# Performance work log

Measured on AMD Instinct MI355X. Metric: run time of the kernel, lower is better.

## Reference

```python
import jax, jax.numpy as jnp
import numpy as np

H = 32        # query heads
D = 128       # head size
HID = H * D   # 4096
B = 4
S = 1024
T = B * S
NSLOTS = 16384
THETA = 10000.0


def _rope(x, cos, sin):
    # x: [T, ..., D]; cos/sin: [T, D//2] -> broadcast over head dims
    half = x.shape[-1] // 2
    while cos.ndim < x.ndim:
        cos = cos[:, None]
        sin = sin[:, None]
    x1, x2 = x[..., :half], x[..., half:]
    return jnp.concatenate([x1 * cos - x2 * sin, x2 * cos + x1 * sin], axis=-1)


def setup_inputs() -> dict:
    key = jax.random.key(0)
    ks = jax.random.split(key, 6)
    hidden_states = jax.random.normal(ks[0], (T, HID), jnp.float32)
    # rotary tables from real positions (repeat per sequence in the batch)
    pos = jnp.tile(jnp.arange(S, dtype=jnp.float32), B)          # [T]
    inv_freq = 1.0 / (THETA ** (jnp.arange(0, D, 2, dtype=jnp.float32) / D))  # [D/2]
    ang = pos[:, None] * inv_freq[None, :]                        # [T, D/2]
    cos, sin = jnp.cos(ang), jnp.sin(ang)
    qkv_w = jax.random.normal(ks[1], (HID, HID + 2 * D), jnp.float32) * 0.02
    qkv_b = jax.random.normal(ks[2], (HID + 2 * D,), jnp.float32) * 0.02
    dense_w = jax.random.normal(ks[3], (HID, HID), jnp.float32) * 0.02
    dense_b = jax.random.normal(ks[4], (HID,), jnp.float32) * 0.02
    k_cache = jnp.zeros((NSLOTS, D), jnp.float32)
    v_cache = jnp.zeros((NSLOTS, D), jnp.float32)
    slots = jnp.arange(T, dtype=jnp.int32)
    return {"hidden_states": hidden_states, "cos": cos, "sin": sin,
            "k_cache": k_cache, "v_cache": v_cache,
            "qkv_w": qkv_w, "qkv_b": qkv_b, "dense_w": dense_w,
            "dense_b": dense_b, "slots": slots, "batch_size": B}


def reference(hidden_states, cos, sin, k_cache, v_cache,
              qkv_w, qkv_b, dense_w, dense_b, slots, batch_size):
    scale = D ** -0.5
    qkv = hidden_states @ qkv_w + qkv_b                  # [T, H*D + 2D]
    q = qkv[:, :HID].reshape(T, H, D)                    # [T,H,D]
    kv = qkv[:, HID:].reshape(T, 2, D)                   # MQA: 1 kv head
    k, v = kv[:, 0], kv[:, 1]                            # [T,D]
    q = _rope(q, cos, sin)
    k = _rope(k, cos, sin)
    # KV-cache scatter store
    k_cache = k_cache.at[slots].set(k)
    v_cache = v_cache.at[slots].set(v)
    # prefill varlen causal attention (uniform lengths -> [B,S] layout)
    qb = q.reshape(batch_size, S, H, D)
    kb = k.reshape(batch_size, S, D)
    vb = v.reshape(batch_size, S, D)
    scores = jnp.einsum('bqhd,bkd->bhqk', qb, kb) * scale
    causal = jnp.tril(jnp.ones((S, S), bool))
    scores = jnp.where(causal[None, None], scores, jnp.float32(-1e30))
    probs = jax.nn.softmax(scores, axis=-1)
    attn = jnp.einsum('bhqk,bkd->bqhd', probs, vb).reshape(T, HID)
    out = attn @ dense_w + dense_b                       # [T, HID]
    return out, k_cache, v_cache
```

## Files before the change

### kernel.cpp

```cpp
#include <hip/hip_runtime.h>

#define H_   32
#define D_   128
#define HID_ 4096
#define B_   4
#define S_   1024
#define T_   4096
#define NSLOTS_ 16384
#define NQKV_ 4352

typedef __attribute__((ext_vector_type(8))) __bf16 bf16x8;
typedef __attribute__((ext_vector_type(4))) __bf16 bf16x4;
typedef __attribute__((ext_vector_type(4))) float  f32x4;

__device__ __forceinline__ void gld_lds16(const __bf16* g, __bf16* l)
{
    __builtin_amdgcn_global_load_lds(
        (const __attribute__((address_space(1))) void*)g,
        (__attribute__((address_space(3))) void*)l, 16, 0, 0);
}

__global__ __launch_bounds__(256) void cast_bf16_kernel(
    const float* __restrict__ in, __bf16* __restrict__ out, int n4)
{
    int i = blockIdx.x * 256 + threadIdx.x;
    if (i < n4) {
        f32x4 v = ((const f32x4*)in)[i];
        bf16x4 o;
        o[0] = (__bf16)v[0]; o[1] = (__bf16)v[1];
        o[2] = (__bf16)v[2]; o[3] = (__bf16)v[3];
        ((bf16x4*)out)[i] = o;
    }
}

__global__ __launch_bounds__(256) void transpose_cast_kernel(
    const float* __restrict__ in, __bf16* __restrict__ out, int R, int C)
{
    __shared__ float tile[32][33];
    int c0 = blockIdx.x * 32, r0 = blockIdx.y * 32;
    int tx = threadIdx.x;
    int ty = threadIdx.y;
#pragma unroll
    for (int j = 0; j < 32; j += 8)
        tile[ty + j][tx] = in[(size_t)(r0 + ty + j) * C + c0 + tx];
    __syncthreads();
#pragma unroll
    for (int j = 0; j < 32; j += 8)
        out[(size_t)(c0 + ty + j) * R + r0 + tx] = (__bf16)tile[tx][ty + j];
}

#define GBK 32
__global__ __launch_bounds__(256) void gemm_bf16_kernel(
    const __bf16* __restrict__ A, const __bf16* __restrict__ Bt,
    const float* __restrict__ bias, float* __restrict__ C,
    int M, int N, int K)
{
    __shared__ __bf16 sA[128][GBK];
    __shared__ __bf16 sB[128][GBK];

    const int tid  = threadIdx.x;
    const int lane = tid & 63;
    const int wave = tid >> 6;
    const int wm   = wave >> 1;
    const int wn   = wave & 1;
    const int col  = lane & 15;
    const int quad = lane >> 4;
    const int bm = blockIdx.y * 128;
    const int bn = blockIdx.x * 128;

    f32x4 acc[4][4];
#pragma unroll
    for (int mt = 0; mt < 4; ++mt)
#pragma unroll
        for (int nt = 0; nt < 4; ++nt)
#pragma unroll
            for (int r = 0; r < 4; ++r) acc[mt][nt][r] = 0.f;

    const int srow = wave * 32 + (lane >> 2);
    const int scol = (lane & 3) * 8;
    const __bf16* gA0 = A  + (size_t)(bm + srow) * K + scol;
    const __bf16* gA1 = A  + (size_t)(bm + srow + 16) * K + scol;
    const __bf16* gB0 = Bt + (size_t)(bn + srow) * K + scol;
    const __bf16* gB1 = Bt + (size_t)(bn + srow + 16) * K + scol;
    __bf16* lA0 = &sA[wave * 32][0];
    __bf16* lA1 = &sA[wave * 32 + 16][0];
    __bf16* lB0 = &sB[wave * 32][0];
    __bf16* lB1 = &sB[wave * 32 + 16][0];

    for (int k0 = 0; k0 < K; k0 += GBK) {
        __syncthreads();
        gld_lds16(gA0 + k0, lA0);
        gld_lds16(gA1 + k0, lA1);
        gld_lds16(gB0 + k0, lB0);
        gld_lds16(gB1 + k0, lB1);
        __syncthreads();

        bf16x8 af[4], bf[4];
#pragma unroll
        for (int mt = 0; mt < 4; ++mt)
            af[mt] = *(const bf16x8*)&sA[wm * 64 + mt * 16 + col][quad * 8];
#pragma unroll
        for (int nt = 0; nt < 4; ++nt)
            bf[nt] = *(const bf16x8*)&sB[wn * 64 + nt * 16 + col][quad * 8];
#pragma unroll
        for (int mt = 0; mt < 4; ++mt)
#pragma unroll
            for (int nt = 0; nt < 4; ++nt)
                acc[mt][nt] = __builtin_amdgcn_mfma_f32_16x16x32_bf16(
                    af[mt], bf[nt], acc[mt][nt], 0, 0, 0);
    }

#pragma unroll
    for (int mt = 0; mt < 4; ++mt) {
#pragma unroll
        for (int nt = 0; nt < 4; ++nt) {
            int r0 = bm + wm * 64 + mt * 16 + quad * 4;
            int c0 = bn + wn * 64 + nt * 16 + col;
            float bv = bias[c0];
#pragma unroll
            for (int r = 0; r < 4; ++r)
                C[(size_t)(r0 + r) * N + c0] = acc[mt][nt][r] + bv;
        }
    }
}

__global__ __launch_bounds__(256) void rope_scatter_kernel(
    const float* __restrict__ qkv, const float* __restrict__ cosb,
    const float* __restrict__ sinb, const int* __restrict__ slots,
    __bf16* __restrict__ q16, __bf16* __restrict__ k16, __bf16* __restrict__ v16,
    float* __restrict__ kcache, float* __restrict__ vcache)
{
    const int t = blockIdx.x;
    const int tid = threadIdx.x;
    const float* row = qkv + (size_t)t * NQKV_;
    const float* cr = cosb + (size_t)t * 64;
    const float* sr = sinb + (size_t)t * 64;
    const int slot = slots[t];

#pragma unroll
    for (int i = 0; i < 8; ++i) {
        int p = tid + 256 * i;
        int h = p >> 6;
        int d = p & 63;
        float x1 = row[h * 128 + d];
        float x2 = row[h * 128 + 64 + d];
        float c = cr[d], s = sr[d];
        q16[(size_t)t * HID_ + h * 128 + d]      = (__bf16)(x1 * c - x2 * s);
        q16[(size_t)t * HID_ + h * 128 + 64 + d] = (__bf16)(x2 * c + x1 * s);
    }
    if (tid < 64) {
        int d = tid;
        float x1 = row[HID_ + d];
        float x2 = row[HID_ + 64 + d];
        float c = cr[d], s = sr[d];
        float o1 = x1 * c - x2 * s;
        float o2 = x2 * c + x1 * s;
        kcache[(size_t)slot * D_ + d]      = o1;
        kcache[(size_t)slot * D_ + 64 + d] = o2;
        k16[(size_t)t * D_ + d]      = (__bf16)o1;
        k16[(size_t)t * D_ + 64 + d] = (__bf16)o2;
    }
    if (tid < 128) {
        float v = row[HID_ + 128 + tid];
        vcache[(size_t)slot * D_ + tid] = v;
        v16[(size_t)t * D_ + tid] = (__bf16)v;
    }
}

__global__ __launch_bounds__(256) void attn_kernel(
    const __bf16* __restrict__ Q, const __bf16* __restrict__ Kc,
    const __bf16* __restrict__ Vc, __bf16* __restrict__ O)
{
    __shared__ __bf16 sK[64][136];
    __shared__ __bf16 sVt[128][72];
    __shared__ __bf16 sP[4][32][72];

    const int h  = blockIdx.y;
    const int b  = blockIdx.z;
    const int tid = threadIdx.x, lane = tid & 63, wave = tid >> 6;
    const int col = lane & 15, quad = lane >> 4;
    const int tbase = b * S_;
    const float scale = 0.08838834764831845f;

    for (int half = 0; half < 2; ++half) {
        const int qt = half ? (7 - blockIdx.x) : blockIdx.x;
        const int qb = qt * 128;

        bf16x8 aq[2][4];
#pragma unroll
        for (int mt = 0; mt < 2; ++mt)
#pragma unroll
            for (int ks = 0; ks < 4; ++ks)
                aq[mt][ks] = *(const bf16x8*)&Q[(size_t)(tbase + qb + wave * 32 + mt * 16 + col) * HID_
                                                + h * 128 + ks * 32 + quad * 8];

        f32x4 o[2][8];
#pragma unroll
        for (int mt = 0; mt < 2; ++mt)
#pragma unroll
            for (int nd = 0; nd < 8; ++nd)
#pragma unroll
                for (int r = 0; r < 4; ++r) o[mt][nd][r] = 0.f;
        float m_i[2][4], l_i[2][4];
#pragma unroll
        for (int mt = 0; mt < 2; ++mt)
#pragma unroll
            for (int r = 0; r < 4; ++r) { m_i[mt][r] = -3.0e38f; l_i[mt][r] = 0.f; }

        const int ntiles = qt * 2 + 2;
        for (int kt = 0; kt < ntiles; ++kt) {
            const int kb = kt * 64;
            __syncthreads();
#pragma unroll
            for (int i = 0; i < 4; ++i) {
                int c = tid + i * 256;
                int srow = c >> 4;
                int d0 = (c & 15) * 8;
                *(uint4*)&sK[srow][d0] = *(const uint4*)&Kc[(size_t)(tbase + kb + srow) * D_ + d0];
            }
#pragma unroll
            for (int i = 0; i < 4; ++i) {
                int c = tid + i * 256;
                int srow = c & 63;
                int d0 = (c >> 6) * 8;
                bf16x8 v = *(const bf16x8*)&Vc[(size_t)(tbase + kb + srow) * D_ + d0];
#pragma unroll
                for (int j = 0; j < 8; ++j) sVt[d0 + j][srow] = v[j];
            }
            __syncthreads();

            f32x4 sc[2][4];
#pragma unroll
            for (int mt = 0; mt < 2; ++mt)
#pragma unroll
                for (int nt = 0; nt < 4; ++nt)
#pragma unroll
                    for (int r = 0; r < 4; ++r) sc[mt][nt][r] = 0.f;
#pragma unroll
            for (int ks = 0; ks < 4; ++ks) {
                bf16x8 bk[4];
#pragma unroll
                for (int nt = 0; nt < 4; ++nt)
                    bk[nt] = *(const bf16x8*)&sK[nt * 16 + col][ks * 32 + quad * 8];
#pragma unroll
                for (int mt = 0; mt < 2; ++mt)
#pragma unroll
                    for (int nt = 0; nt < 4; ++nt)
                        sc[mt][nt] = __builtin_amdgcn_mfma_f32_16x16x32_bf16(
                            aq[mt][ks], bk[nt], sc[mt][nt], 0, 0, 0);
            }

#pragma unroll
            for (int mt = 0; mt < 2; ++mt) {
#pragma unroll
                for (int r = 0; r < 4; ++r) {
                    int qrow = qb + wave * 32 + mt * 16 + quad * 4 + r;
#pragma unroll
                    for (int nt = 0; nt < 4; ++nt) {
                        float v = sc[mt][nt][r] * scale;
                        int kcol = kb + nt * 16 + col;
                        sc[mt][nt][r] = (kcol > qrow) ? -3.0e38f : v;
                    }
                    float mx = sc[mt][0][r];
#pragma unroll
                    for (int nt = 1; nt < 4; ++nt) mx = fmaxf(mx, sc[mt][nt][r]);
#pragma unroll
                    for (int x = 1; x < 16; x <<= 1) mx = fmaxf(mx, __shfl_xor(mx, x, 64));
                    float mnew = fmaxf(m_i[mt][r], mx);
                    float alpha = __expf(m_i[mt][r] - mnew);
                    m_i[mt][r] = mnew;
                    float rs = 0.f;
#pragma unroll
                    for (int nt = 0; nt < 4; ++nt) {
                        float p = __expf(sc[mt][nt][r] - mnew);
                        sc[mt][nt][r] = p;
                        rs += p;
                    }
#pragma unroll
                    for (int x = 1; x < 16; x <<= 1) rs += __shfl_xor(rs, x, 64);
                    l_i[mt][r] = l_i[mt][r] * alpha + rs;
#pragma unroll
                    for (int nd = 0; nd < 8; ++nd) o[mt][nd][r] *= alpha;
                }
            }

#pragma unroll
            for (int mt = 0; mt < 2; ++mt)
#pragma unroll
                for (int nt = 0; nt < 4; ++nt)
#pragma unroll
                    for (int r = 0; r < 4; ++r)
                        sP[wave][mt * 16 + quad * 4 + r][nt * 16 + col] = (__bf16)sc[mt][nt][r];

#pragma unroll
            for (int ks2 = 0; ks2 < 2; ++ks2) {
                bf16x8 ap[2];
#pragma unroll
                for (int mt = 0; mt < 2; ++mt)
                    ap[mt] = *(const bf16x8*)&sP[wave][mt * 16 + col][ks2 * 32 + quad * 8];
#pragma unroll
                for (int nd = 0; nd < 8; ++nd) {
                    bf16x8 bv = *(const bf16x8*)&sVt[nd * 16 + col][ks2 * 32 + quad * 8];
#pragma unroll
                    for (int mt = 0; mt < 2; ++mt)
                        o[mt][nd] = __builtin_amdgcn_mfma_f32_16x16x32_bf16(
                            ap[mt], bv, o[mt][nd], 0, 0, 0);
                }
            }
        }

#pragma unroll
        for (int mt = 0; mt < 2; ++mt) {
#pragma unroll
            for (int r = 0; r < 4; ++r) {
                int t = tbase + qb + wave * 32 + mt * 16 + quad * 4 + r;
                float inv_l = 1.f / l_i[mt][r];
#pragma unroll
                for (int nd = 0; nd < 8; ++nd)
                    O[(size_t)t * HID_ + h * 128 + nd * 16 + col] = (__bf16)(o[mt][nd][r] * inv_l);
            }
        }
    }
}

extern "C" void kernel_launch(void* const* d_in, const int* in_sizes, int n_in,
                              void* d_out, int out_size, void* d_ws, size_t ws_size,
                              hipStream_t stream)
{
    const float* hidden  = (const float*)d_in[0];
    const float* cosb    = (const float*)d_in[1];
    const float* sinb    = (const float*)d_in[2];
    const float* kc_in   = (const float*)d_in[3];
    const float* vc_in   = (const float*)d_in[4];
    const float* qkv_w   = (const float*)d_in[5];
    const float* qkv_b   = (const float*)d_in[6];
    const float* dense_w = (const float*)d_in[7];
    const float* dense_b = (const float*)d_in[8];
    const int*   slots   = (const int*)d_in[9];

    float* out    = (float*)d_out;
    float* kc_out = out + (size_t)T_ * HID_;
    float* vc_out = kc_out + (size_t)NSLOTS_ * D_;

    char* ws = (char*)d_ws;
    __bf16* A16 = (__bf16*)(ws);
    __bf16* W1T = (__bf16*)(ws + 33554432);
    float*  QKV = (float*)(ws + 69206016);
    __bf16* W2T = (__bf16*)(ws + 69206016);
    __bf16* Q16 = (__bf16*)d_out;
    __bf16* K16 = (__bf16*)((char*)d_out + 33554432);
    __bf16* V16 = (__bf16*)((char*)d_out + 34603008);

    cast_bf16_kernel<<<(T_ * HID_ / 4 + 255) / 256, 256, 0, stream>>>(hidden, A16, T_ * HID_ / 4);
    transpose_cast_kernel<<<dim3(NQKV_ / 32, HID_ / 32), dim3(32, 8), 0, stream>>>(qkv_w, W1T, HID_, NQKV_);
    gemm_bf16_kernel<<<dim3(NQKV_ / 128, T_ / 128), 256, 0, stream>>>(A16, W1T, qkv_b, QKV, T_, NQKV_, HID_);
    hipMemcpyAsync(kc_out, kc_in, (size_t)NSLOTS_ * D_ * 4, hipMemcpyDeviceToDevice, stream);
    hipMemcpyAsync(vc_out, vc_in, (size_t)NSLOTS_ * D_ * 4, hipMemcpyDeviceToDevice, stream);
    rope_scatter_kernel<<<T_, 256, 0, stream>>>(QKV, cosb, sinb, slots, Q16, K16, V16, kc_out, vc_out);
    transpose_cast_kernel<<<dim3(HID_ / 32, HID_ / 32), dim3(32, 8), 0, stream>>>(dense_w, W2T, HID_, HID_);
    attn_kernel<<<dim3(4, H_, B_), 256, 0, stream>>>(Q16, K16, V16, A16);
    gemm_bf16_kernel<<<dim3(HID_ / 128, T_ / 128), 256, 0, stream>>>(A16, W2T, dense_b, out, T_, HID_, HID_);
}
```

Before: 823.1 us.

## Replace 128x128 GEMM with pipelined 256x256 tile kernel using swizzled LDS

Both projection GEMMs now use a 512-thread kernel with 256x256 output tiles and 64-wide K steps. Global-to-LDS loads are double-buffered and staged in quarter chunks ahead of compute, with an XOR swizzle to avoid LDS bank conflicts. Explicit waitcnt, barriers and setprio interleave loads with MFMA work. The aim is more data reuse per byte loaded and latency hiding, at the cost of more registers (32 accumulators), 64KB LDS, and fragile hand-written synchronisation.

```diff
diff --git a/kernel.cpp b/kernel.cpp
--- a/kernel.cpp
+++ b/kernel.cpp
@@ -49,77 +49,128 @@
         out[(size_t)(c0 + ty + j) * R + r0 + tx] = (__bf16)tile[tx][ty + j];
 }
 
-#define GBK 32
-__global__ __launch_bounds__(256) void gemm_bf16_kernel(
+
+#define SB()    __builtin_amdgcn_sched_barrier(0)
+#define BAR()   __builtin_amdgcn_s_barrier()
+#define LGKM0() asm volatile("s_waitcnt lgkmcnt(0)" ::: "memory")
+
+#define LOAD_A(MH, KK)                                                          \
+    _Pragma("unroll")                                                           \
+    for (int m = 0; m < 4; ++m)                                                 \
+        afr[m] = *(const bf16x8*)&lds[buf][KK][(wm * 128 + ((MH)*4 + m) * 16 + col) * 32 + pbE];
+
+#define MFMA_QUAD(MH, KK)                                                       \
+    __builtin_amdgcn_s_setprio(1);                                              \
+    _Pragma("unroll")                                                           \
+    for (int m = 0; m < 4; ++m) {                                               \
+        _Pragma("unroll")                                                       \
+        for (int n = 0; n < 4; ++n)                                             \
+            acc[(MH)*4 + m][n] = __builtin_amdgcn_mfma_f32_16x16x32_bf16(       \
+                afr[m], bfr[KK][n], acc[(MH)*4 + m][n], 0, 0, 0);               \
+    }                                                                           \
+    __builtin_amdgcn_s_setprio(0);
+
+__global__ __launch_bounds__(512, 2) void gemm256_kernel(
     const __bf16* __restrict__ A, const __bf16* __restrict__ Bt,
     const float* __restrict__ bias, float* __restrict__ C,
     int M, int N, int K)
 {
-    __shared__ __bf16 sA[128][GBK];
-    __shared__ __bf16 sB[128][GBK];
+    __shared__ __bf16 lds[2][4][8192];
 
     const int tid  = threadIdx.x;
     const int lane = tid & 63;
     const int wave = tid >> 6;
-    const int wm   = wave >> 1;
-    const int wn   = wave & 1;
+    const int wm   = wave >> 2;
+    const int wn   = wave & 3;
     const int col  = lane & 15;
     const int quad = lane >> 4;
-    const int bm = blockIdx.y * 128;
-    const int bn = blockIdx.x * 128;
-
-    f32x4 acc[4][4];
-#pragma unroll
-    for (int mt = 0; mt < 4; ++mt)
-#pragma unroll
-        for (int nt = 0; nt < 4; ++nt)
-#pragma unroll
-            for (int r = 0; r < 4; ++r) acc[mt][nt][r] = 0.f;
-
-    const int srow = wave * 32 + (lane >> 2);
-    const int scol = (lane & 3) * 8;
-    const __bf16* gA0 = A  + (size_t)(bm + srow) * K + scol;
-    const __bf16* gA1 = A  + (size_t)(bm + srow + 16) * K + scol;
-    const __bf16* gB0 = Bt + (size_t)(bn + srow) * K + scol;
-    const __bf16* gB1 = Bt + (size_t)(bn + srow + 16) * K + scol;
-    __bf16* lA0 = &sA[wave * 32][0];
-    __bf16* lA1 = &sA[wave * 32 + 16][0];
-    __bf16* lB0 = &sB[wave * 32][0];
-    __bf16* lB1 = &sB[wave * 32 + 16][0];
-
-    for (int k0 = 0; k0 < K; k0 += GBK) {
-        __syncthreads();
-        gld_lds16(gA0 + k0, lA0);
-        gld_lds16(gA1 + k0, lA1);
-        gld_lds16(gB0 + k0, lB0);
-        gld_lds16(gB1 + k0, lB1);
-        __syncthreads();
-
-        bf16x8 af[4], bf[4];
-#pragma unroll
-        for (int mt = 0; mt < 4; ++mt)
-            af[mt] = *(const bf16x8*)&sA[wm * 64 + mt * 16 + col][quad * 8];
-#pragma unroll
-        for (int nt = 0; nt < 4; ++nt)
-            bf[nt] = *(const bf16x8*)&sB[wn * 64 + nt * 16 + col][quad * 8];
-#pragma unroll
-        for (int mt = 0; mt < 4; ++mt)
-#pragma unroll
-            for (int nt = 0; nt < 4; ++nt)
-                acc[mt][nt] = __builtin_amdgcn_mfma_f32_16x16x32_bf16(
-                    af[mt], bf[nt], acc[mt][nt], 0, 0, 0);
-    }
-
-#pragma unroll
-    for (int mt = 0; mt < 4; ++mt) {
-#pragma unroll
-        for (int nt = 0; nt < 4; ++nt) {
-            int r0 = bm + wm * 64 + mt * 16 + quad * 4;
-            int c0 = bn + wn * 64 + nt * 16 + col;
-            float bv = bias[c0];
+    const int pbE  = (quad ^ ((lane >> 1) & 3)) * 8;
+    const int bm   = blockIdx.y * 256;
+    const int bn   = blockIdx.x * 256;
+    const int nk   = K >> 6;
+    const int nitems = nk << 2;
+
+    const int sR = wave * 32 + (lane >> 2);
+    const int sb = ((lane & 3) ^ ((lane >> 3) & 3)) * 8;
+    const __bf16* gA = A  + (size_t)(bm + sR) * K + sb;
+    const __bf16* gB = Bt + (size_t)(bn + sR) * K + sb;
+
+    f32x4 acc[8][4];
+#pragma unroll
+    for (int m = 0; m < 8; ++m)
+#pragma unroll
+        for (int n = 0; n < 4; ++n)
+#pragma unroll
+            for (int r = 0; r < 4; ++r) acc[m][n][r] = 0.f;
+
+    auto stage = [&](int idx) {
+        if (idx >= nitems) return;
+        const int j   = idx >> 2;
+        const int sel = idx & 3;
+        const int reg = sel ^ 2;
+        const __bf16* g = (sel & 2) ? gA : gB;
+        const size_t koff = (size_t)j * 64 + (size_t)(sel & 1) * 32;
+        __bf16* l = &lds[j & 1][reg][wave * 1024];
+        gld_lds16(g + koff, l);
+        gld_lds16(g + koff + (size_t)16 * K, l + 512);
+    };
+
+    stage(0); stage(1); stage(2); stage(3);
+    asm volatile("s_waitcnt vmcnt(4)" ::: "memory");
+    stage(4); stage(5); stage(6);
+    asm volatile("s_waitcnt vmcnt(6)" ::: "memory");
+    BAR();
+    SB();
+
+    for (int k = 0; k < nk; ++k) {
+        const int buf = k & 1;
+        bf16x8 bfr[2][4];
+        bf16x8 afr[4];
+
+#pragma unroll
+        for (int kk = 0; kk < 2; ++kk)
+#pragma unroll
+            for (int n = 0; n < 4; ++n)
+                bfr[kk][n] = *(const bf16x8*)&lds[buf][2 + kk][(wn * 64 + n * 16 + col) * 32 + pbE];
+        LOAD_A(0, 0)
+        stage(4 * k + 7);
+        SB(); BAR(); LGKM0(); SB();
+        MFMA_QUAD(0, 0)
+        SB(); BAR(); SB();
+
+        LOAD_A(1, 0)
+        stage(4 * k + 8);
+        SB(); BAR(); LGKM0(); SB();
+        MFMA_QUAD(1, 0)
+        SB(); BAR(); SB();
+
+        LOAD_A(0, 1)
+        stage(4 * k + 9);
+        SB(); BAR(); LGKM0(); SB();
+        MFMA_QUAD(0, 1)
+        SB(); BAR(); SB();
+
+        LOAD_A(1, 1)
+        stage(4 * k + 10);
+        SB(); BAR(); LGKM0(); SB();
+        MFMA_QUAD(1, 1)
+        SB();
+        if (k < nk - 2) asm volatile("s_waitcnt vmcnt(6)" ::: "memory");
+        else            asm volatile("s_waitcnt vmcnt(0)" ::: "memory");
+        BAR();
+        SB();
+    }
+
+#pragma unroll
+    for (int m = 0; m < 8; ++m) {
+#pragma unroll
+        for (int n = 0; n < 4; ++n) {
+            const int r0 = bm + wm * 128 + m * 16 + quad * 4;
+            const int c0 = bn + wn * 64 + n * 16 + col;
+            const float bv = bias[c0];
 #pragma unroll
             for (int r = 0; r < 4; ++r)
-                C[(size_t)(r0 + r) * N + c0] = acc[mt][nt][r] + bv;
+                C[(size_t)(r0 + r) * N + c0] = acc[m][n][r] + bv;
         }
     }
 }
@@ -353,11 +404,11 @@
 
     cast_bf16_kernel<<<(T_ * HID_ / 4 + 255) / 256, 256, 0, stream>>>(hidden, A16, T_ * HID_ / 4);
     transpose_cast_kernel<<<dim3(NQKV_ / 32, HID_ / 32), dim3(32, 8), 0, stream>>>(qkv_w, W1T, HID_, NQKV_);
-    gemm_bf16_kernel<<<dim3(NQKV_ / 128, T_ / 128), 256, 0, stream>>>(A16, W1T, qkv_b, QKV, T_, NQKV_, HID_);
+    gemm256_kernel<<<dim3(NQKV_ / 256, T_ / 256), 512, 0, stream>>>(A16, W1T, qkv_b, QKV, T_, NQKV_, HID_);
     hipMemcpyAsync(kc_out, kc_in, (size_t)NSLOTS_ * D_ * 4, hipMemcpyDeviceToDevice, stream);
     hipMemcpyAsync(vc_out, vc_in, (size_t)NSLOTS_ * D_ * 4, hipMemcpyDeviceToDevice, stream);
     rope_scatter_kernel<<<T_, 256, 0, stream>>>(QKV, cosb, sinb, slots, Q16, K16, V16, kc_out, vc_out);
     transpose_cast_kernel<<<dim3(HID_ / 32, HID_ / 32), dim3(32, 8), 0, stream>>>(dense_w, W2T, HID_, HID_);
     attn_kernel<<<dim3(4, H_, B_), 256, 0, stream>>>(Q16, K16, V16, A16);
-    gemm_bf16_kernel<<<dim3(HID_ / 128, T_ / 128), 256, 0, stream>>>(A16, W2T, dense_b, out, T_, HID_, HID_);
-}
+    gemm256_kernel<<<dim3(HID_ / 256, T_ / 256), 512, 0, stream>>>(A16, W2T, dense_b, out, T_, HID_, HID_);
+}
```

Result: faster. 744.5 us (-9.6%).

## Double-buffer GEMM LDS tiles with swizzle and XCD-aware block remap

Applied to the files above, without the earlier changes.

Rewrites the bf16 GEMM to double-buffer its shared-memory tiles, issuing the global-to-LDS loads for step k+2 while MFMAs run on step k, with explicit waitcnt and barrier scheduling. It adds an XOR swizzle on the LDS layout to cut bank conflicts, and remaps the 1D grid so consecutive tiles are spread across the 8 XCDs for better L2 locality. The aim is to hide global-load latency and the two full barriers per K step of the old loop. The hand-placed inline asm waits and sched barriers are fragile, and the grid remap assumes the block count divides by 8.

```diff
diff --git a/kernel.cpp b/kernel.cpp
--- a/kernel.cpp
+++ b/kernel.cpp
@@ -20,6 +20,18 @@
         (__attribute__((address_space(3))) void*)l, 16, 0, 0);
 }
 
+__device__ __forceinline__ bf16x8 ds_read_b128a(const __bf16* p)
+{
+    bf16x8 r;
+    unsigned a = (unsigned)(size_t)(const __attribute__((address_space(3))) __bf16*)p;
+    asm volatile("ds_read_b128 %0, %1" : "=&v"(r) : "v"(a));
+    return r;
+}
+
+#define SB()    __builtin_amdgcn_sched_barrier(0)
+#define BAR()   __builtin_amdgcn_s_barrier()
+#define LGKM0() asm volatile("s_waitcnt lgkmcnt(0)" ::: "memory")
+
 __global__ __launch_bounds__(256) void cast_bf16_kernel(
     const float* __restrict__ in, __bf16* __restrict__ out, int n4)
 {
@@ -49,14 +61,13 @@
         out[(size_t)(c0 + ty + j) * R + r0 + tx] = (__bf16)tile[tx][ty + j];
 }
 
-#define GBK 32
-__global__ __launch_bounds__(256) void gemm_bf16_kernel(
+__global__ __launch_bounds__(256, 4) void gemm128_kernel(
     const __bf16* __restrict__ A, const __bf16* __restrict__ Bt,
     const float* __restrict__ bias, float* __restrict__ C,
     int M, int N, int K)
 {
-    __shared__ __bf16 sA[128][GBK];
-    __shared__ __bf16 sB[128][GBK];
+    __shared__ __bf16 sA[2][128 * 32];
+    __shared__ __bf16 sB[2][128 * 32];
 
     const int tid  = threadIdx.x;
     const int lane = tid & 63;
@@ -65,61 +76,81 @@
     const int wn   = wave & 1;
     const int col  = lane & 15;
     const int quad = lane >> 4;
-    const int bm = blockIdx.y * 128;
-    const int bn = blockIdx.x * 128;
+    const int pbE  = (quad ^ ((lane >> 1) & 3)) * 8;
+
+    const int nbx  = N >> 7;
+    const int nwg  = gridDim.x;
+    const int cpx  = nwg >> 3;
+    const int wg   = (blockIdx.x & 7) * cpx + (blockIdx.x >> 3);
+    const int bm   = (wg / nbx) * 128;
+    const int bn   = (wg % nbx) * 128;
+    const int nt   = K >> 5;
+
+    const int sR = wave * 32 + (lane >> 2);
+    const int sb = ((lane & 3) ^ ((lane >> 3) & 3)) * 8;
+    const __bf16* gA = A  + (size_t)(bm + sR) * K + sb;
+    const __bf16* gB = Bt + (size_t)(bn + sR) * K + sb;
 
     f32x4 acc[4][4];
 #pragma unroll
-    for (int mt = 0; mt < 4; ++mt)
-#pragma unroll
-        for (int nt = 0; nt < 4; ++nt)
-#pragma unroll
-            for (int r = 0; r < 4; ++r) acc[mt][nt][r] = 0.f;
-
-    const int srow = wave * 32 + (lane >> 2);
-    const int scol = (lane & 3) * 8;
-    const __bf16* gA0 = A  + (size_t)(bm + srow) * K + scol;
-    const __bf16* gA1 = A  + (size_t)(bm + srow + 16) * K + scol;
-    const __bf16* gB0 = Bt + (size_t)(bn + srow) * K + scol;
-    const __bf16* gB1 = Bt + (size_t)(bn + srow + 16) * K + scol;
-    __bf16* lA0 = &sA[wave * 32][0];
-    __bf16* lA1 = &sA[wave * 32 + 16][0];
-    __bf16* lB0 = &sB[wave * 32][0];
-    __bf16* lB1 = &sB[wave * 32 + 16][0];
-
-    for (int k0 = 0; k0 < K; k0 += GBK) {
-        __syncthreads();
-        gld_lds16(gA0 + k0, lA0);
-        gld_lds16(gA1 + k0, lA1);
-        gld_lds16(gB0 + k0, lB0);
-        gld_lds16(gB1 + k0, lB1);
-        __syncthreads();
-
-        bf16x8 af[4], bf[4];
-#pragma unroll
-        for (int mt = 0; mt < 4; ++mt)
-            af[mt] = *(const bf16x8*)&sA[wm * 64 + mt * 16 + col][quad * 8];
-#pragma unroll
-        for (int nt = 0; nt < 4; ++nt)
-            bf[nt] = *(const bf16x8*)&sB[wn * 64 + nt * 16 + col][quad * 8];
-#pragma unroll
-        for (int mt = 0; mt < 4; ++mt)
-#pragma unroll
-            for (int nt = 0; nt < 4; ++nt)
-                acc[mt][nt] = __builtin_amdgcn_mfma_f32_16x16x32_bf16(
-                    af[mt], bf[nt], acc[mt][nt], 0, 0, 0);
-    }
-
-#pragma unroll
-    for (int mt = 0; mt < 4; ++mt) {
-#pragma unroll
-        for (int nt = 0; nt < 4; ++nt) {
-            int r0 = bm + wm * 64 + mt * 16 + quad * 4;
-            int c0 = bn + wn * 64 + nt * 16 + col;
-            float bv = bias[c0];
+    for (int m = 0; m < 4; ++m)
+#pragma unroll
+        for (int n = 0; n < 4; ++n)
+#pragma unroll
+            for (int r = 0; r < 4; ++r) acc[m][n][r] = 0.f;
+
+    auto stage = [&](int j) {
+        if (j >= nt) return;
+        const size_t ko = (size_t)j * 32;
+        __bf16* la = &sA[j & 1][wave * 1024];
+        __bf16* lb = &sB[j & 1][wave * 1024];
+        gld_lds16(gA + ko, la);
+        gld_lds16(gA + ko + (size_t)16 * K, la + 512);
+        gld_lds16(gB + ko, lb);
+        gld_lds16(gB + ko + (size_t)16 * K, lb + 512);
+    };
+
+    stage(0); stage(1);
+    asm volatile("s_waitcnt vmcnt(4)" ::: "memory");
+    BAR(); SB();
+
+    for (int k = 0; k < nt; ++k) {
+        const int buf = k & 1;
+        bf16x8 afr[4], bfr[4];
+#pragma unroll
+        for (int m = 0; m < 4; ++m)
+            afr[m] = ds_read_b128a(&sA[buf][(wm * 64 + m * 16 + col) * 32 + pbE]);
+#pragma unroll
+        for (int n = 0; n < 4; ++n)
+            bfr[n] = ds_read_b128a(&sB[buf][(wn * 64 + n * 16 + col) * 32 + pbE]);
+        SB();
+        LGKM0(); SB();
+        BAR(); SB();
+        stage(k + 2);
+        __builtin_amdgcn_s_setprio(1);
+#pragma unroll
+        for (int m = 0; m < 4; ++m)
+#pragma unroll
+            for (int n = 0; n < 4; ++n)
+                acc[m][n] = __builtin_amdgcn_mfma_f32_16x16x32_bf16(
+                    afr[m], bfr[n], acc[m][n], 0, 0, 0);
+        __builtin_amdgcn_s_setprio(0);
+        SB();
+        if (k < nt - 2) asm volatile("s_waitcnt vmcnt(4)" ::: "memory");
+        else            asm volatile("s_waitcnt vmcnt(0)" ::: "memory");
+        BAR(); SB();
+    }
+
+#pragma unroll
+    for (int m = 0; m < 4; ++m) {
+#pragma unroll
+        for (int n = 0; n < 4; ++n) {
+            const int r0 = bm + wm * 64 + m * 16 + quad * 4;
+            const int c0 = bn + wn * 64 + n * 16 + col;
+            const float bv = bias[c0];
 #pragma unroll
             for (int r = 0; r < 4; ++r)
-                C[(size_t)(r0 + r) * N + c0] = acc[mt][nt][r] + bv;
+                C[(size_t)(r0 + r) * N + c0] = acc[m][n][r] + bv;
         }
     }
 }
@@ -353,11 +384,11 @@
 
     cast_bf16_kernel<<<(T_ * HID_ / 4 + 255) / 256, 256, 0, stream>>>(hidden, A16, T_ * HID_ / 4);
     transpose_cast_kernel<<<dim3(NQKV_ / 32, HID_ / 32), dim3(32, 8), 0, stream>>>(qkv_w, W1T, HID_, NQKV_);
-    gemm_bf16_kernel<<<dim3(NQKV_ / 128, T_ / 128), 256, 0, stream>>>(A16, W1T, qkv_b, QKV, T_, NQKV_, HID_);
+    gemm128_kernel<<<(T_ / 128) * (NQKV_ / 128), 256, 0, stream>>>(A16, W1T, qkv_b, QKV, T_, NQKV_, HID_);
     hipMemcpyAsync(kc_out, kc_in, (size_t)NSLOTS_ * D_ * 4, hipMemcpyDeviceToDevice, stream);
     hipMemcpyAsync(vc_out, vc_in, (size_t)NSLOTS_ * D_ * 4, hipMemcpyDeviceToDevice, stream);
     rope_scatter_kernel<<<T_, 256, 0, stream>>>(QKV, cosb, sinb, slots, Q16, K16, V16, kc_out, vc_out);
     transpose_cast_kernel<<<dim3(HID_ / 32, HID_ / 32), dim3(32, 8), 0, stream>>>(dense_w, W2T, HID_, HID_);
     attn_kernel<<<dim3(4, H_, B_), 256, 0, stream>>>(Q16, K16, V16, A16);
-    gemm_bf16_kernel<<<dim3(HID_ / 128, T_ / 128), 256, 0, stream>>>(A16, W2T, dense_b, out, T_, HID_, HID_);
-}
+    gemm128_kernel<<<(T_ / 128) * (HID_ / 128), 256, 0, stream>>>(A16, W2T, dense_b, out, T_, HID_, HID_);
+}
```

Result: faster. 784.6 us (-4.7%).
